# Performance work log

Hardware: AMD Instinct MI355X
Metric: run time of the kernel (lower is better)

## Reference

```python
import jax, jax.numpy as jnp
import numpy as np

DILATIONS = [32, 64, 128, 256, 512, 1024]
HID = 50


def gru_scan(X, W, U, b):
    # X: [T, N, D] time-major. Keras GRUCell, reset_after=True (default).
    # W: [D, 3H], U: [H, 3H], b: [2, 3H] (input bias, recurrent bias).
    H = U.shape[0]
    bi, br = b[0], b[1]
    Xg = jnp.einsum('tnd,dh->tnh', X, W) + bi  # precompute input gates [T, N, 3H]
    h0 = jnp.zeros((X.shape[1], H), X.dtype)

    def step(h, xg):
        rec = h @ U + br
        z = jax.nn.sigmoid(xg[:, :H] + rec[:, :H])
        r = jax.nn.sigmoid(xg[:, H:2 * H] + rec[:, H:2 * H])
        hh = jnp.tanh(xg[:, 2 * H:] + r * rec[:, 2 * H:])
        hn = z * h + (1.0 - z) * hh
        return hn, hn

    _, Y = jax.lax.scan(step, h0, Xg)
    return Y  # [T, N, H]


def drnn_layer(X, rate, W, U, b):
    # X: [T, B, D]. Faithful to source: concat rate consecutive timesteps into
    # the batch dim, run GRU over dn steps, then split(axis=1)+concat(axis=0).
    T, B, D = X.shape
    dn = -(-T // rate)
    pad = dn * rate - T
    if pad:
        X = jnp.pad(X, ((0, pad), (0, 0), (0, 0)))
    Xd = X.reshape(dn, rate * B, D)          # dilated_inputs, stacked time-major
    Y = gru_scan(Xd, W, U, b)                # [dn, rate*B, H]
    H = Y.shape[-1]
    # split axis=1 into `rate` pieces of [dn, B, H], concat axis=0 -> [rate*dn, B, H]
    Yr = Y.reshape(dn, rate, B, H).transpose(1, 0, 2, 3).reshape(rate * dn, B, H)
    return Yr[:T]


def setup_inputs() -> dict:
    key = jax.random.key(0)
    ks = jax.random.split(key, 16)
    B, T, D, H, C = 64, 2048, 128, HID, 41
    s = 0.05
    inp = {
        'x': jax.random.normal(ks[0], (B, T, D), jnp.float32),
        # layer 0 (input dim D)
        'gru_W0': jax.random.normal(ks[1], (D, 3 * H), jnp.float32) * s,
        'gru_U0': jax.random.normal(ks[2], (H, 3 * H), jnp.float32) * s,
        'gru_b0': jnp.zeros((2, 3 * H), jnp.float32),
        # layers 1..5 (input dim H), stacked
        'gru_W': jax.random.normal(ks[3], (5, H, 3 * H), jnp.float32) * s,
        'gru_U': jax.random.normal(ks[4], (5, H, 3 * H), jnp.float32) * s,
        'gru_b': jnp.zeros((5, 2, 3 * H), jnp.float32),
        # head: dense2 takes concat of last dilations[0]=32 outputs -> 1600 feats
        'dense2_W': jax.random.normal(ks[5], (H * DILATIONS[0], H * DILATIONS[0]), jnp.float32) * s,
        'dense2_b': jnp.zeros((H * DILATIONS[0],), jnp.float32),
        'cls_W': jax.random.normal(ks[6], (H * DILATIONS[0], C), jnp.float32) * s,
        'cls_b': jnp.zeros((C,), jnp.float32),
    }
    return inp


def reference(x, gru_W0, gru_U0, gru_b0, gru_W, gru_U, gru_b,
              dense2_W, dense2_b, cls_W, cls_b):
    X = jnp.transpose(x, (1, 0, 2))  # time-major [T, B, D]
    X = drnn_layer(X, DILATIONS[0], gru_W0, gru_U0, gru_b0)
    for i in range(5):
        X = drnn_layer(X, DILATIONS[i + 1], gru_W[i], gru_U[i], gru_b[i])
    B = X.shape[1]
    # dilations[0] != 1 branch: concat last 32 timestep outputs along features
    feats = X[-DILATIONS[0]:].transpose(1, 0, 2).reshape(B, -1)  # [B, 1600]
    h = jax.nn.relu(feats @ dense2_W + dense2_b)
    logits = h @ cls_W + cls_b
    return jax.nn.softmax(logits, axis=-1)
```

## Files before the change

### kernel.cpp

```cpp
#include <hip/hip_runtime.h>
#include <math.h>

#define HH   50
#define GG   150
#define XGS  152
#define TTT  2048
#define NB   64
#define MTOT (TTT*NB)
#define D0   128

static __device__ __forceinline__ float sigm(float x) {
    return 1.f / (1.f + __expf(-x));
}
static __device__ __forceinline__ float tanh_f(float x) {
    return 1.f - 2.f / (__expf(2.f * x) + 1.f);
}

static __device__ __forceinline__ void fma4(float4& a, float s, const float4& w) {
    a.x += s * w.x; a.y += s * w.y; a.z += s * w.z; a.w += s * w.w;
}

static __device__ __forceinline__ float bcast(float v, int k) {
    return __uint_as_float(__builtin_amdgcn_readlane(__float_as_uint(v), k));
}

__global__ __launch_bounds__(256) void proj0_kernel(
    const float* __restrict__ x,
    const float* __restrict__ W,
    const float* __restrict__ bias,
    float* __restrict__ xg)
{
    __shared__ float xs[128][36];
    __shared__ float Wp[32][32];
    const int tid  = threadIdx.x;
    const int m0   = blockIdx.x * 128;
    const int c0   = blockIdx.y * 32;
    const int rowq = tid >> 3;
    const int colq = tid & 7;

    float4 acc[4];
    #pragma unroll
    for (int j = 0; j < 4; ++j) acc[j] = make_float4(0.f, 0.f, 0.f, 0.f);

    for (int q = 0; q < 4; ++q) {
        if (q) __syncthreads();
        for (int i = tid; i < 128 * 8; i += 256) {
            int r = i >> 3, k4 = (i & 7) * 4;
            int row = m0 + r, t = row >> 6, b = row & 63;
            *(float4*)&xs[r][k4] =
                *(const float4*)&x[((size_t)b * TTT + t) * D0 + q * 32 + k4];
        }
        for (int i = tid; i < 32 * 32; i += 256) {
            int k = i >> 5, c = i & 31, gc = c0 + c;
            Wp[k][c] = (gc < GG) ? W[(q * 32 + k) * GG + gc] : 0.f;
        }
        __syncthreads();
        const float* xr0 = xs[rowq * 4 + 0];
        const float* xr1 = xs[rowq * 4 + 1];
        const float* xr2 = xs[rowq * 4 + 2];
        const float* xr3 = xs[rowq * 4 + 3];
        for (int k = 0; k < 32; k += 4) {
            float4 w0 = *(const float4*)&Wp[k + 0][colq * 4];
            float4 w1 = *(const float4*)&Wp[k + 1][colq * 4];
            float4 w2 = *(const float4*)&Wp[k + 2][colq * 4];
            float4 w3 = *(const float4*)&Wp[k + 3][colq * 4];
            float4 x0 = *(const float4*)&xr0[k];
            float4 x1 = *(const float4*)&xr1[k];
            float4 x2 = *(const float4*)&xr2[k];
            float4 x3 = *(const float4*)&xr3[k];
            fma4(acc[0], x0.x, w0); fma4(acc[0], x0.y, w1);
            fma4(acc[0], x0.z, w2); fma4(acc[0], x0.w, w3);
            fma4(acc[1], x1.x, w0); fma4(acc[1], x1.y, w1);
            fma4(acc[1], x1.z, w2); fma4(acc[1], x1.w, w3);
            fma4(acc[2], x2.x, w0); fma4(acc[2], x2.y, w1);
            fma4(acc[2], x2.z, w2); fma4(acc[2], x2.w, w3);
            fma4(acc[3], x3.x, w0); fma4(acc[3], x3.y, w1);
            fma4(acc[3], x3.z, w2); fma4(acc[3], x3.w, w3);
        }
    }
    const int cc = c0 + colq * 4;
    if (cc <= XGS - 4) {
        float4 bv = *(const float4*)&bias[cc];
        #pragma unroll
        for (int j = 0; j < 4; ++j) {
            float4 o;
            o.x = acc[j].x + bv.x; o.y = acc[j].y + bv.y;
            o.z = acc[j].z + bv.z; o.w = acc[j].w + bv.w;
            *(float4*)&xg[(size_t)(m0 + rowq * 4 + j) * XGS + cc] = o;
        }
    }
}

template<int WPB, int RPW>
__global__ __launch_bounds__(WPB * 64) void gru_reg(
    const float* __restrict__ xg,
    const float* __restrict__ U,
    const float* __restrict__ bias,
    float* __restrict__ Xout,
    int dn, int Nbatch, int ngroups)
{
    constexpr int R = WPB * RPW;
    __shared__ __align__(16) float Ut[HH][HH][4];

    const int tid  = threadIdx.x;
    const int wav  = tid >> 6;
    const int lane = tid & 63;

    for (int i = tid; i < HH * HH; i += WPB * 64)
        Ut[i / HH][i - (i / HH) * HH][3] = 0.f;
    for (int i = tid; i < HH * GG; i += WPB * 64) {
        int k = i / GG, cc = i - k * GG;
        Ut[k][cc % HH][cc / HH] = U[i];
    }
    __syncthreads();

    const int c  = lane;
    const int cb = (c < HH) ? c : HH - 1;

    const float bz  = bias[GG + cb];
    const float brr = bias[GG + HH + cb];
    const float bh  = bias[GG + 2 * HH + cb];

    for (int grp = blockIdx.x; grp < ngroups; grp += gridDim.x) {
        const int row0 = grp * R + wav * RPW;
        float h[RPW];
        #pragma unroll
        for (int j = 0; j < RPW; ++j) h[j] = 0.f;
        size_t obase[RPW];
        #pragma unroll
        for (int j = 0; j < RPW; ++j) {
            int nr = row0 + j;
            obase[j] = ((size_t)((nr >> 6) * dn) * NB + (nr & 63)) * HH + cb;
        }
        const float* gb = xg + (size_t)row0 * XGS;

        float px[RPW], pr[RPW], ph[RPW];
        #pragma unroll
        for (int j = 0; j < RPW; ++j) {
            const float* g = gb + (size_t)j * XGS;
            px[j] = g[cb]; pr[j] = g[HH + cb]; ph[j] = g[2 * HH + cb];
        }

        for (int s = 0; s < dn; ++s) {
            const int sn = (s + 1 < dn) ? s + 1 : s;
            float nx[RPW], nrr[RPW], nh[RPW];
            #pragma unroll
            for (int j = 0; j < RPW; ++j) {
                const float* g = gb + ((size_t)sn * Nbatch + j) * XGS;
                nx[j] = g[cb]; nrr[j] = g[HH + cb]; nh[j] = g[2 * HH + cb];
            }
            float az[RPW], ar[RPW], ah[RPW];
            #pragma unroll
            for (int j = 0; j < RPW; ++j) { az[j] = bz; ar[j] = brr; ah[j] = bh; }
            #pragma unroll 5
            for (int k = 0; k < HH; ++k) {
                float4 w = *(const float4*)&Ut[k][c < HH ? c : 0][0];
                #pragma unroll
                for (int j = 0; j < RPW; ++j) {
                    float hk = bcast(h[j], k);
                    az[j] += hk * w.x;
                    ar[j] += hk * w.y;
                    ah[j] += hk * w.z;
                }
            }
            #pragma unroll
            for (int j = 0; j < RPW; ++j) {
                float z  = sigm(px[j] + az[j]);
                float r  = sigm(pr[j] + ar[j]);
                float hh = tanh_f(ph[j] + r * ah[j]);
                float hn = z * h[j] + (1.f - z) * hh;
                h[j] = hn;
                if (c < HH) Xout[obase[j] + (size_t)s * NB * HH] = hn;
            }
            #pragma unroll
            for (int j = 0; j < RPW; ++j) { px[j] = nx[j]; pr[j] = nrr[j]; ph[j] = nh[j]; }
        }
    }
}

template<int WPB, int RPW>
__global__ __launch_bounds__(WPB * 64) void gru_fused(
    const float* __restrict__ Xin,
    const float* __restrict__ W,
    const float* __restrict__ U,
    const float* __restrict__ bias,
    float* __restrict__ Xout,
    int dn, int Nbatch, int ngroups)
{
    constexpr int R = WPB * RPW;
    __shared__ __align__(16) float Ut[HH][HH][4];
    __shared__ __align__(16) float Wt[HH][HH][4];

    const int tid  = threadIdx.x;
    const int wav  = tid >> 6;
    const int lane = tid & 63;

    for (int i = tid; i < HH * HH; i += WPB * 64) {
        Ut[i / HH][i - (i / HH) * HH][3] = 0.f;
        Wt[i / HH][i - (i / HH) * HH][3] = 0.f;
    }
    for (int i = tid; i < HH * GG; i += WPB * 64) {
        int k = i / GG, cc = i - k * GG;
        Ut[k][cc % HH][cc / HH] = U[i];
        Wt[k][cc % HH][cc / HH] = W[i];
    }
    __syncthreads();

    const int c  = lane;
    const int cb = (c < HH) ? c : HH - 1;

    const float biz = bias[cb];
    const float bir = bias[HH + cb];
    const float bih = bias[2 * HH + cb];
    const float brz = bias[GG + cb];
    const float brr = bias[GG + HH + cb];
    const float brh = bias[GG + 2 * HH + cb];

    for (int grp = blockIdx.x; grp < ngroups; grp += gridDim.x) {
        const int row0 = grp * R + wav * RPW;
        float h[RPW];
        #pragma unroll
        for (int j = 0; j < RPW; ++j) h[j] = 0.f;
        size_t obase[RPW];
        #pragma unroll
        for (int j = 0; j < RPW; ++j) {
            int nr = row0 + j;
            obase[j] = ((size_t)((nr >> 6) * dn) * NB + (nr & 63)) * HH + cb;
        }
        const float* gb = Xin + (size_t)row0 * HH;

        float px[RPW];
        #pragma unroll
        for (int j = 0; j < RPW; ++j) px[j] = gb[(size_t)j * HH + cb];

        for (int s = 0; s < dn; ++s) {
            const int sn = (s + 1 < dn) ? s + 1 : s;
            float nx[RPW];
            #pragma unroll
            for (int j = 0; j < RPW; ++j)
                nx[j] = gb[((size_t)sn * Nbatch + j) * HH + cb];

            float gz[RPW], gr[RPW], gh[RPW];
            #pragma unroll
            for (int j = 0; j < RPW; ++j) { gz[j] = biz; gr[j] = bir; gh[j] = bih; }
            #pragma unroll 5
            for (int k = 0; k < HH; ++k) {
                float4 w = *(const float4*)&Wt[k][c < HH ? c : 0][0];
                #pragma unroll
                for (int j = 0; j < RPW; ++j) {
                    float xk = bcast(px[j], k);
                    gz[j] += xk * w.x;
                    gr[j] += xk * w.y;
                    gh[j] += xk * w.z;
                }
            }
            float az[RPW], ar[RPW], ah[RPW];
            #pragma unroll
            for (int j = 0; j < RPW; ++j) { az[j] = brz; ar[j] = brr; ah[j] = brh; }
            #pragma unroll 5
            for (int k = 0; k < HH; ++k) {
                float4 w = *(const float4*)&Ut[k][c < HH ? c : 0][0];
                #pragma unroll
                for (int j = 0; j < RPW; ++j) {
                    float hk = bcast(h[j], k);
                    az[j] += hk * w.x;
                    ar[j] += hk * w.y;
                    ah[j] += hk * w.z;
                }
            }
            #pragma unroll
            for (int j = 0; j < RPW; ++j) {
                float z  = sigm(gz[j] + az[j]);
                float r  = sigm(gr[j] + ar[j]);
                float hh = tanh_f(gh[j] + r * ah[j]);
                float hn = z * h[j] + (1.f - z) * hh;
                h[j] = hn;
                if (c < HH) Xout[obase[j] + (size_t)s * NB * HH] = hn;
            }
            #pragma unroll
            for (int j = 0; j < RPW; ++j) px[j] = nx[j];
        }
    }
}

__global__ __launch_bounds__(256) void dense2_kernel(
    const float* __restrict__ X,
    const float* __restrict__ W2,
    float* __restrict__ part)
{
    __shared__ float fs[8][100];
    const int tid = threadIdx.x;
    const int c  = blockIdx.x * 256 + tid;
    const int r0 = blockIdx.y * 8;
    const int kz = blockIdx.z;
    for (int i = tid; i < 8 * 100; i += 256) {
        int r = i / 100, fl = i - r * 100;
        int f = kz * 100 + fl, j = f / HH, k = f - j * HH;
        fs[r][fl] = X[((size_t)(TTT - 32 + j) * NB + (r0 + r)) * HH + k];
    }
    __syncthreads();
    if (c < 1600) {
        float a[8] = {0, 0, 0, 0, 0, 0, 0, 0};
        const float* w = W2 + (size_t)kz * 100 * 1600 + c;
        for (int fl = 0; fl < 100; ++fl) {
            float wv = w[(size_t)fl * 1600];
            #pragma unroll
            for (int r = 0; r < 8; ++r) a[r] += fs[r][fl] * wv;
        }
        #pragma unroll
        for (int r = 0; r < 8; ++r)
            part[((size_t)kz * NB + r0 + r) * 1600 + c] = a[r];
    }
}

__global__ __launch_bounds__(256) void cls_kernel(
    const float* __restrict__ part,
    const float* __restrict__ b2,
    const float* __restrict__ Wc,
    const float* __restrict__ bc,
    float* __restrict__ out)
{
    __shared__ float hrow[1600];
    __shared__ float lg[41];
    __shared__ float red[2];
    const int b = blockIdx.x;
    const int t = threadIdx.x;
    for (int i = t; i < 1600; i += 256) {
        float s = b2[i];
        #pragma unroll 4
        for (int kz = 0; kz < 16; ++kz)
            s += part[((size_t)kz * NB + b) * 1600 + i];
        hrow[i] = s > 0.f ? s : 0.f;
    }
    __syncthreads();
    if (t < 41) {
        float acc = bc[t];
        for (int f = 0; f < 1600; ++f) acc += hrow[f] * Wc[f * 41 + t];
        lg[t] = acc;
    }
    __syncthreads();
    if (t == 0) {
        float mx = lg[0];
        for (int i = 1; i < 41; ++i) mx = fmaxf(mx, lg[i]);
        red[0] = mx;
    }
    __syncthreads();
    if (t < 41) lg[t] = expf(lg[t] - red[0]);
    __syncthreads();
    if (t == 0) {
        float sm = 0.f;
        for (int i = 0; i < 41; ++i) sm += lg[i];
        red[1] = 1.f / sm;
    }
    __syncthreads();
    if (t < 41) out[b * 41 + t] = lg[t] * red[1];
}

extern "C" void kernel_launch(void* const* d_in, const int* in_sizes, int n_in,
                              void* d_out, int out_size, void* d_ws, size_t ws_size,
                              hipStream_t stream)
{
    const float* x   = (const float*)d_in[0];
    const float* W0  = (const float*)d_in[1];
    const float* U0  = (const float*)d_in[2];
    const float* b0  = (const float*)d_in[3];
    const float* Ws  = (const float*)d_in[4];
    const float* Us  = (const float*)d_in[5];
    const float* bs  = (const float*)d_in[6];
    const float* W2  = (const float*)d_in[7];
    const float* b2  = (const float*)d_in[8];
    const float* Wc  = (const float*)d_in[9];
    const float* bc  = (const float*)d_in[10];

    float* region1 = (float*)d_ws;
    float* xg   = region1;
    float* bufB = region1;
    float* part = region1 + (size_t)MTOT * HH;
    float* bufA = region1 + (size_t)MTOT * XGS;

    static const int rates[6] = {32, 64, 128, 256, 512, 1024};

    proj0_kernel<<<dim3(MTOT / 128, 5), 256, 0, stream>>>(x, W0, b0, xg);
    {
        int dn = TTT / rates[0], Nbatch = rates[0] * NB;
        int ngroups = Nbatch / 8;
        int grid = ngroups < 512 ? ngroups : 512;
        gru_reg<4, 2><<<grid, 256, 0, stream>>>(xg, U0, b0, bufA, dn, Nbatch, ngroups);
    }

    const float* cur = bufA;
    for (int l = 1; l < 6; ++l) {
        const float* Wl = Ws + (size_t)(l - 1) * HH * GG;
        const float* Ul = Us + (size_t)(l - 1) * HH * GG;
        const float* bl = bs + (size_t)(l - 1) * 2 * GG;
        int rate = rates[l];
        int Nbatch = rate * NB;
        int dn = TTT / rate;
        float* dst = (cur == bufA) ? bufB : bufA;
        if (l <= 2) {
            int ngroups = Nbatch / 16;
            int grid = ngroups < 512 ? ngroups : 512;
            gru_fused<4, 4><<<grid, 256, 0, stream>>>(cur, Wl, Ul, bl, dst, dn, Nbatch, ngroups);
        } else {
            int ngroups = Nbatch / 32;
            int grid = ngroups < 512 ? ngroups : 512;
            gru_fused<4, 8><<<grid, 256, 0, stream>>>(cur, Wl, Ul, bl, dst, dn, Nbatch, ngroups);
        }
        cur = dst;
    }

    dense2_kernel<<<dim3(7, 8, 16), 256, 0, stream>>>(cur, W2, part);
    cls_kernel<<<NB, 256, 0, stream>>>(part, b2, Wc, bc, (float*)d_out);
}
```

Baseline: 1.031 ms.

## Stage hidden and input vectors in LDS and fuse GRU gate matvec loops

Adds gru_fused2, which writes each wave's h and x vectors transposed into shared memory. The recurrent and input projections are then computed in one merged k-loop that reads vectors from LDS, instead of using per-element readlane broadcasts in two separate loops. The W and U weights are repacked into a float4 plus float2 layout so one iteration supplies all six gate weights. Rows per wave are also retuned: layer 1 now uses 2 and the later layers use 4. The risks are extra LDS traffic and occupancy, and correctness depends on each wave reading back its own LDS writes in order without a barrier.

```diff
diff --git a/kernel.cpp b/kernel.cpp
--- a/kernel.cpp
+++ b/kernel.cpp
@@ -179,7 +179,7 @@
 }
 
 template<int WPB, int RPW>
-__global__ __launch_bounds__(WPB * 64) void gru_fused(
+__global__ __launch_bounds__(WPB * 64) void gru_fused2(
     const float* __restrict__ Xin,
     const float* __restrict__ W,
     const float* __restrict__ U,
@@ -187,27 +187,33 @@
     float* __restrict__ Xout,
     int dn, int Nbatch, int ngroups)
 {
-    constexpr int R = WPB * RPW;
-    __shared__ __align__(16) float Ut[HH][HH][4];
-    __shared__ __align__(16) float Wt[HH][HH][4];
+    constexpr int R  = WPB * RPW;
+    constexpr int RS = R + 4;
+    __shared__ __align__(16) float UWs[HH][HH][4];
+    __shared__ __align__(16) float W2s[HH][HH][2];
+    __shared__ __align__(16) float hsT[HH][RS];
+    __shared__ __align__(16) float xsT[HH][RS];
 
     const int tid  = threadIdx.x;
     const int wav  = tid >> 6;
     const int lane = tid & 63;
 
     for (int i = tid; i < HH * HH; i += WPB * 64) {
-        Ut[i / HH][i - (i / HH) * HH][3] = 0.f;
-        Wt[i / HH][i - (i / HH) * HH][3] = 0.f;
-    }
-    for (int i = tid; i < HH * GG; i += WPB * 64) {
-        int k = i / GG, cc = i - k * GG;
-        Ut[k][cc % HH][cc / HH] = U[i];
-        Wt[k][cc % HH][cc / HH] = W[i];
-    }
-    __syncthreads();
-
-    const int c  = lane;
-    const int cb = (c < HH) ? c : HH - 1;
+        int k = i / HH, cc = i - k * HH;
+        const float* u = U + k * GG;
+        const float* w = W + k * GG;
+        UWs[k][cc][0] = u[cc];
+        UWs[k][cc][1] = u[HH + cc];
+        UWs[k][cc][2] = u[2 * HH + cc];
+        UWs[k][cc][3] = w[cc];
+        W2s[k][cc][0] = w[HH + cc];
+        W2s[k][cc][1] = w[2 * HH + cc];
+    }
+    __syncthreads();
+
+    const int c   = lane;
+    const int cb  = (c < HH) ? c : HH - 1;
+    const bool act = (c < HH);
 
     const float biz = bias[cb];
     const float bir = bias[HH + cb];
@@ -218,54 +224,63 @@
 
     for (int grp = blockIdx.x; grp < ngroups; grp += gridDim.x) {
         const int row0 = grp * R + wav * RPW;
-        float h[RPW];
-        #pragma unroll
-        for (int j = 0; j < RPW; ++j) h[j] = 0.f;
+        float h[RPW], px[RPW];
         size_t obase[RPW];
         #pragma unroll
         for (int j = 0; j < RPW; ++j) {
+            h[j] = 0.f;
             int nr = row0 + j;
             obase[j] = ((size_t)((nr >> 6) * dn) * NB + (nr & 63)) * HH + cb;
         }
+        if (act) {
+            #pragma unroll
+            for (int j = 0; j < RPW; ++j) hsT[c][wav * RPW + j] = 0.f;
+        }
         const float* gb = Xin + (size_t)row0 * HH;
-
-        float px[RPW];
         #pragma unroll
         for (int j = 0; j < RPW; ++j) px[j] = gb[(size_t)j * HH + cb];
 
         for (int s = 0; s < dn; ++s) {
+            if (act) {
+                #pragma unroll
+                for (int j = 0; j < RPW; ++j) xsT[c][wav * RPW + j] = px[j];
+            }
             const int sn = (s + 1 < dn) ? s + 1 : s;
             float nx[RPW];
             #pragma unroll
             for (int j = 0; j < RPW; ++j)
                 nx[j] = gb[((size_t)sn * Nbatch + j) * HH + cb];
 
-            float gz[RPW], gr[RPW], gh[RPW];
-            #pragma unroll
-            for (int j = 0; j < RPW; ++j) { gz[j] = biz; gr[j] = bir; gh[j] = bih; }
+            float gz[RPW], gr[RPW], gh[RPW], az[RPW], ar[RPW], ah[RPW];
+            #pragma unroll
+            for (int j = 0; j < RPW; ++j) {
+                gz[j] = biz; gr[j] = bir; gh[j] = bih;
+                az[j] = brz; ar[j] = brr; ah[j] = brh;
+            }
             #pragma unroll 5
             for (int k = 0; k < HH; ++k) {
-                float4 w = *(const float4*)&Wt[k][c < HH ? c : 0][0];
+                float4 uw = *(const float4*)&UWs[k][cb][0];
+                float2 w2 = *(const float2*)&W2s[k][cb][0];
+                float hv[RPW], xv[RPW];
+                if constexpr (RPW == 4) {
+                    float4 t  = *(const float4*)&hsT[k][wav * RPW];
+                    hv[0] = t.x; hv[1] = t.y; hv[2] = t.z; hv[3] = t.w;
+                    float4 u2 = *(const float4*)&xsT[k][wav * RPW];
+                    xv[0] = u2.x; xv[1] = u2.y; xv[2] = u2.z; xv[3] = u2.w;
+                } else {
+                    float2 t  = *(const float2*)&hsT[k][wav * RPW];
+                    hv[0] = t.x; hv[1] = t.y;
+                    float2 u2 = *(const float2*)&xsT[k][wav * RPW];
+                    xv[0] = u2.x; xv[1] = u2.y;
+                }
                 #pragma unroll
                 for (int j = 0; j < RPW; ++j) {
-                    float xk = bcast(px[j], k);
-                    gz[j] += xk * w.x;
-                    gr[j] += xk * w.y;
-                    gh[j] += xk * w.z;
-                }
-            }
-            float az[RPW], ar[RPW], ah[RPW];
-            #pragma unroll
-            for (int j = 0; j < RPW; ++j) { az[j] = brz; ar[j] = brr; ah[j] = brh; }
-            #pragma unroll 5
-            for (int k = 0; k < HH; ++k) {
-                float4 w = *(const float4*)&Ut[k][c < HH ? c : 0][0];
-                #pragma unroll
-                for (int j = 0; j < RPW; ++j) {
-                    float hk = bcast(h[j], k);
-                    az[j] += hk * w.x;
-                    ar[j] += hk * w.y;
-                    ah[j] += hk * w.z;
+                    az[j] += hv[j] * uw.x;
+                    ar[j] += hv[j] * uw.y;
+                    ah[j] += hv[j] * uw.z;
+                    gz[j] += xv[j] * uw.w;
+                    gr[j] += xv[j] * w2.x;
+                    gh[j] += xv[j] * w2.y;
                 }
             }
             #pragma unroll
@@ -275,7 +290,10 @@
                 float hh = tanh_f(gh[j] + r * ah[j]);
                 float hn = z * h[j] + (1.f - z) * hh;
                 h[j] = hn;
-                if (c < HH) Xout[obase[j] + (size_t)s * NB * HH] = hn;
+                if (act) {
+                    hsT[c][wav * RPW + j] = hn;
+                    Xout[obase[j] + (size_t)s * NB * HH] = hn;
+                }
             }
             #pragma unroll
             for (int j = 0; j < RPW; ++j) px[j] = nx[j];
@@ -397,14 +415,14 @@
         int Nbatch = rate * NB;
         int dn = TTT / rate;
         float* dst = (cur == bufA) ? bufB : bufA;
-        if (l <= 2) {
+        if (l == 1) {
+            int ngroups = Nbatch / 8;
+            int grid = ngroups < 512 ? ngroups : 512;
+            gru_fused2<4, 2><<<grid, 256, 0, stream>>>(cur, Wl, Ul, bl, dst, dn, Nbatch, ngroups);
+        } else {
             int ngroups = Nbatch / 16;
             int grid = ngroups < 512 ? ngroups : 512;
-            gru_fused<4, 4><<<grid, 256, 0, stream>>>(cur, Wl, Ul, bl, dst, dn, Nbatch, ngroups);
-        } else {
-            int ngroups = Nbatch / 32;
-            int grid = ngroups < 512 ? ngroups : 512;
-            gru_fused<4, 8><<<grid, 256, 0, stream>>>(cur, Wl, Ul, bl, dst, dn, Nbatch, ngroups);
+            gru_fused2<4, 4><<<grid, 256, 0, stream>>>(cur, Wl, Ul, bl, dst, dn, Nbatch, ngroups);
         }
         cur = dst;
     }
```

Measured after the change: 890.7 us. 13.6% less time.
